# Kernel tuning notes

Measured on AMD Instinct MI355X. Metric: run time of the kernel, lower is better.

The kernel has to match this reference:

```python
import jax, jax.numpy as jnp
import numpy as np

NB_POOLS = 256


def setup_inputs() -> dict:
    key = jax.random.key(0)
    x = jax.random.normal(key, (32, 32, 32, 512), dtype=jnp.float32)
    return {"x": x}


def reference(x) -> jnp.ndarray:
    B, R, C, F = x.shape
    nb_maps = R * C
    x3 = x.reshape(B, nb_maps, F)
    # self-correlation: (B, nb_maps, nb_maps), normalized by feature count
    corr = jnp.einsum('bmf,bnf->bmn', x3, x3) / F
    corr = corr.reshape(B, R, C, nb_maps)
    # percentile ranks into the descending-sorted correlation values
    ranks = jnp.round(jnp.linspace(1.0, nb_maps - 1, NB_POOLS)).astype(jnp.int32)
    # full descending sort along last axis (matches tf.nn.top_k k=nb_maps)
    x_sort = -jnp.sort(-corr, axis=-1)
    x_pool = x_sort[..., ranks]  # (B, R, C, NB_POOLS)
    return x_pool
```

## Files before the change

### kernel.cpp

```cpp
#include <hip/hip_runtime.h>


#define NMAPS 1024
#define FDIM 512
#define TM 16
#define NT 256

typedef __attribute__((ext_vector_type(8))) short short8_t;
typedef __attribute__((ext_vector_type(4))) float f32x4;
typedef _Float16 h2 __attribute__((ext_vector_type(2)));

__device__ __forceinline__ h2 h2min(h2 a, h2 b) { return __builtin_elementwise_min(a, b); }
__device__ __forceinline__ h2 h2max(h2 a, h2 b) { return __builtin_elementwise_max(a, b); }

__device__ __forceinline__ h2 h2swap(h2 v) {
  union { h2 h; unsigned u; } x;
  x.h = v;
  x.u = (x.u >> 16) | (x.u << 16);
  return x.h;
}

__device__ __forceinline__ h2 h2shfl_xor(h2 v, int m) {
  union { h2 h; int i; } u;
  u.h = v;
  u.i = __shfl_xor(u.i, m, 64);
  return u.h;
}

template<int K>
__device__ __forceinline__ void bitonic_stage(h2 w8[8], int lane) {
  const bool laneDesc = (K >= 16) ? ((lane & (K >> 4)) == 0) : true;
#pragma unroll
  for (int j = 512; j >= 16; j >>= 1) {
    if (j > (K >> 1)) continue;
    const int m = j >> 4;
    const bool keepmax = (((lane & m) == 0) == laneDesc);
#pragma unroll
    for (int u = 0; u < 8; ++u) {
      h2 p = h2shfl_xor(w8[u], m);
      h2 mn = h2min(w8[u], p), mx = h2max(w8[u], p);
      w8[u] = keepmax ? mx : mn;
    }
  }
#pragma unroll
  for (int j = 8; j >= 2; j >>= 1) {
    if (j > (K >> 1)) continue;
    const int jw = j >> 1;
#pragma unroll
    for (int u = 0; u < 8; ++u) {
      if ((u & jw) == 0) {
        const int v = u | jw;
        const bool desc = (K <= 8) ? (((2 * u) & K) == 0) : laneDesc;
        h2 mn = h2min(w8[u], w8[v]), mx = h2max(w8[u], w8[v]);
        w8[u] = desc ? mx : mn;
        w8[v] = desc ? mn : mx;
      }
    }
  }
#pragma unroll
  for (int u = 0; u < 8; ++u) {
    const bool desc = (K <= 8) ? (((2 * u) & K) == 0) : laneDesc;
    h2 s = h2swap(w8[u]);
    h2 mn = h2min(w8[u], s), mx = h2max(w8[u], s);
    h2 rd = (h2){mx[0], mn[1]};
    h2 ra = (h2){mn[0], mx[1]};
    w8[u] = desc ? rd : ra;
  }
}

__device__ __forceinline__ void run_bitonic(h2 w8[8], int lane) {
  bitonic_stage<2>(w8, lane);
  bitonic_stage<4>(w8, lane);
  bitonic_stage<8>(w8, lane);
  bitonic_stage<16>(w8, lane);
  bitonic_stage<32>(w8, lane);
  bitonic_stage<64>(w8, lane);
  bitonic_stage<128>(w8, lane);
  bitonic_stage<256>(w8, lane);
  bitonic_stage<512>(w8, lane);
  bitonic_stage<1024>(w8, lane);
}

__global__ __launch_bounds__(256) void cvt_bf16_kernel(const float* __restrict__ x,
                                                       short* __restrict__ xw, int n8) {
  int i = blockIdx.x * 256 + threadIdx.x;
  if (i >= n8) return;
  const float4* x4 = reinterpret_cast<const float4*>(x);
  float4 a = x4[i * 2], c = x4[i * 2 + 1];
  float f[8] = {a.x, a.y, a.z, a.w, c.x, c.y, c.z, c.w};
  union { short8_t v; short s[8]; } o;
#pragma unroll
  for (int j = 0; j < 8; ++j) {
    unsigned u = __float_as_uint(f[j]);
    u += 0x7fffu + ((u >> 16) & 1u);
    o.s[j] = (short)(u >> 16);
  }
  reinterpret_cast<short8_t*>(xw)[i] = o.v;
}

__global__ __launch_bounds__(NT) void corr_gemm_tiled(const short* __restrict__ xw,
                                                      unsigned* __restrict__ corrW) {
  __shared__ short Asm[128 * 32];
  __shared__ short Bsm[128 * 32];
  const int tid = threadIdx.x;
  const int b = blockIdx.y;
  const int it = blockIdx.x >> 3, jt = blockIdx.x & 7;
  const int i0 = it * 128, j0 = jt * 128;
  const int lane = tid & 63;
  const int wid = tid >> 6;
  const int lr = lane & 15;
  const int kg = lane >> 4;
  const int wr = wid >> 1, wc = wid & 1;
  const short* Xb = xw + (size_t)b * NMAPS * FDIM;

  f32x4 acc[4][4];
#pragma unroll
  for (int fm = 0; fm < 4; ++fm)
#pragma unroll
    for (int fn = 0; fn < 4; ++fn) acc[fm][fn] = (f32x4){0.f, 0.f, 0.f, 0.f};

  for (int kt = 0; kt < 16; ++kt) {
    __syncthreads();
#pragma unroll
    for (int rp = 0; rp < 2; ++rp) {
      const int idx = rp * 256 + tid;
      const int r = idx >> 2, s = idx & 3;
      const short* gA = Xb + (size_t)(i0 + r) * FDIM + kt * 32 + s * 8;
      const short* gB = Xb + (size_t)(j0 + r) * FDIM + kt * 32 + s * 8;
      __builtin_amdgcn_global_load_lds(
          (const __attribute__((address_space(1))) unsigned*)gA,
          (__attribute__((address_space(3))) unsigned*)(Asm + idx * 8), 16, 0, 0);
      __builtin_amdgcn_global_load_lds(
          (const __attribute__((address_space(1))) unsigned*)gB,
          (__attribute__((address_space(3))) unsigned*)(Bsm + idx * 8), 16, 0, 0);
    }
    __syncthreads();

    short8_t a[4], bf[4];
#pragma unroll
    for (int fm = 0; fm < 4; ++fm)
      a[fm] = *reinterpret_cast<const short8_t*>(Asm + (wr * 64 + fm * 16 + lr) * 32 + kg * 8);
#pragma unroll
    for (int fn = 0; fn < 4; ++fn)
      bf[fn] = *reinterpret_cast<const short8_t*>(Bsm + (wc * 64 + fn * 16 + lr) * 32 + kg * 8);
#pragma unroll
    for (int fm = 0; fm < 4; ++fm)
#pragma unroll
      for (int fn = 0; fn < 4; ++fn)
        acc[fm][fn] = __builtin_amdgcn_mfma_f32_16x16x32_bf16(bf[fn], a[fm], acc[fm][fn], 0, 0, 0);
  }

#pragma unroll
  for (int fm = 0; fm < 4; ++fm) {
    const size_t roww = ((size_t)b * NMAPS + i0 + wr * 64 + fm * 16 + lr) * 512;
#pragma unroll
    for (int fn = 0; fn < 4; ++fn) {
      h2 lo = (h2){(_Float16)(acc[fm][fn][0] * (1.f / FDIM)),
                   (_Float16)(acc[fm][fn][1] * (1.f / FDIM))};
      h2 hi = (h2){(_Float16)(acc[fm][fn][2] * (1.f / FDIM)),
                   (_Float16)(acc[fm][fn][3] * (1.f / FDIM))};
      const int wq = (j0 + wc * 64 + fn * 16 + kg * 4) >> 1;
      union { h2 h[2]; uint2 u; } pk;
      pk.h[0] = lo; pk.h[1] = hi;
      *reinterpret_cast<uint2*>(corrW + roww + wq) = pk.u;
    }
  }
}

__global__ __launch_bounds__(256) void sort_rows_kernel(const unsigned* __restrict__ corrW,
                                                        float* __restrict__ out) {
  const int tid = threadIdx.x;
  const int lane = tid & 63;
  const int row = blockIdx.x * 4 + (tid >> 6);
  const uint4* r4 = reinterpret_cast<const uint4*>(corrW + (size_t)row * 512);

  h2 w8[8];
  {
    union { uint4 u; h2 h[4]; } a, c;
    a.u = r4[lane * 2];
    c.u = r4[lane * 2 + 1];
    w8[0] = a.h[0]; w8[1] = a.h[1]; w8[2] = a.h[2]; w8[3] = a.h[3];
    w8[4] = c.h[0]; w8[5] = c.h[1]; w8[6] = c.h[2]; w8[7] = c.h[3];
  }

  run_bitonic(w8, lane);

  float* orow = out + (size_t)row * 256;
#pragma unroll
  for (int u = 0; u < 8; ++u) {
#pragma unroll
    for (int hh = 0; hh < 2; ++hh) {
      const int i = lane * 16 + 2 * u + hh;
      const int p = (int)rint((double)(i - 1) * (255.0 / 1022.0));
      const int rk = (int)rint(1.0 + (double)p * (1022.0 / 255.0));
      if (rk == i) orow[p] = (float)w8[u][hh];
    }
  }
}

__global__ __launch_bounds__(NT) void selfcorr_mfma_kernel(const short* __restrict__ xw,
                                                           float* __restrict__ out) {
  __shared__ alignas(16) h2 SH[TM * 512];
  const int tid = threadIdx.x;
  const int b = blockIdx.y;
  const int m0 = blockIdx.x * TM;
  const int lane = tid & 63;
  const int wid = tid >> 6;
  const int lr = lane & 15;
  const int kg = lane >> 4;
  const int wc = wid * 256;
  const short* Xb = xw + (size_t)b * NMAPS * FDIM;

  f32x4 acc[16];
#pragma unroll
  for (int t = 0; t < 16; ++t) acc[t] = (f32x4){0.f, 0.f, 0.f, 0.f};

  for (int kk = 0; kk < 16; ++kk) {
    const short8_t* base = reinterpret_cast<const short8_t*>(Xb + kk * 32 + kg * 8);
    short8_t afrag = base[(size_t)(m0 + lr) * 64];
    short8_t bfrag[16];
#pragma unroll
    for (int t = 0; t < 16; ++t) bfrag[t] = base[(size_t)(wc + t * 16 + lr) * 64];
#pragma unroll
    for (int t = 0; t < 16; ++t)
      acc[t] = __builtin_amdgcn_mfma_f32_16x16x32_bf16(bfrag[t], afrag, acc[t], 0, 0, 0);
  }

  {
    const int xorv = (lr & 7) << 2;
#pragma unroll
    for (int t = 0; t < 16; ++t) {
      h2 lo = (h2){(_Float16)(acc[t][0] * (1.f / FDIM)), (_Float16)(acc[t][1] * (1.f / FDIM))};
      h2 hi = (h2){(_Float16)(acc[t][2] * (1.f / FDIM)), (_Float16)(acc[t][3] * (1.f / FDIM))};
      const int W = (wc >> 1) + t * 8 + kg * 2;
      const int phys = lr * 512 + (W ^ xorv);
      union { h2 h[2]; uint2 u; } pk;
      pk.h[0] = lo; pk.h[1] = hi;
      *reinterpret_cast<uint2*>(&SH[phys]) = pk.u;
    }
  }
  __syncthreads();

  const int rowbase = wid * 4;
  for (int rr = rowbase; rr < rowbase + 4; ++rr) {
    const int rx = (rr & 7) << 2;
    h2 w8[8];
#pragma unroll
    for (int q = 0; q < 2; ++q) {
      const int p4 = rr * 512 + ((lane * 8 + q * 4) ^ rx);
      union { uint4 u; h2 h[4]; } un;
      un.u = *reinterpret_cast<const uint4*>(&SH[p4]);
      w8[q * 4 + 0] = un.h[0]; w8[q * 4 + 1] = un.h[1];
      w8[q * 4 + 2] = un.h[2]; w8[q * 4 + 3] = un.h[3];
    }
    run_bitonic(w8, lane);
#pragma unroll
    for (int q = 0; q < 2; ++q) {
      const int p4 = rr * 512 + ((lane * 8 + q * 4) ^ rx);
      union { uint4 u; h2 h[4]; } un;
      un.h[0] = w8[q * 4 + 0]; un.h[1] = w8[q * 4 + 1];
      un.h[2] = w8[q * 4 + 2]; un.h[3] = w8[q * 4 + 3];
      *reinterpret_cast<uint4*>(&SH[p4]) = un.u;
    }
  }
  __builtin_amdgcn_wave_barrier();

#pragma unroll
  for (int i = 0; i < 16; ++i) {
    const int rr = rowbase + (i >> 2);
    const int p = lane + ((i & 3) << 6);
    const int rank = (int)rint(1.0 + (double)p * (1022.0 / 255.0));
    const int Wr = (rank >> 1) ^ ((rr & 7) << 2);
    h2 hv = SH[rr * 512 + Wr];
    out[((size_t)(b * NMAPS + m0 + rr) << 8) + p] = (float)hv[rank & 1];
  }
}

__device__ __forceinline__ int sw4(int row, int c4) {
  return (row << 8) | (c4 ^ ((c4 >> 3) & 7));
}
__device__ __forceinline__ void ce(float& a, float& b, bool desc) {
  float mn = fminf(a, b);
  float mx = fmaxf(a, b);
  a = desc ? mx : mn;
  b = desc ? mn : mx;
}

__global__ __launch_bounds__(NT) void selfcorr_pool_kernel(const float* __restrict__ x,
                                                           float* __restrict__ out) {
  __shared__ float lds[TM * NMAPS];
  float4* S4 = reinterpret_cast<float4*>(lds);
  const int tid = threadIdx.x;
  const int b = blockIdx.y;
  const int m0 = blockIdx.x * TM;
  const float4* Xb = reinterpret_cast<const float4*>(x) + (size_t)b * NMAPS * (FDIM / 4);

  float4* A4 = reinterpret_cast<float4*>(lds);
#pragma unroll
  for (int idx = tid; idx < TM * (FDIM / 4); idx += NT) {
    A4[idx] = Xb[(m0 + (idx >> 7)) * 128 + (idx & 127)];
  }
  __syncthreads();

  float acc[TM][4];
#pragma unroll
  for (int m = 0; m < TM; ++m)
#pragma unroll
    for (int j = 0; j < 4; ++j) acc[m][j] = 0.0f;

  float4 nb0 = Xb[(tid + 0) * 128];
  float4 nb1 = Xb[(tid + 256) * 128];
  float4 nb2 = Xb[(tid + 512) * 128];
  float4 nb3 = Xb[(tid + 768) * 128];
  for (int k4 = 0; k4 < 128; ++k4) {
    float4 b0 = nb0, b1 = nb1, b2 = nb2, b3 = nb3;
    const int kn = (k4 < 127) ? (k4 + 1) : 127;
    nb0 = Xb[(tid + 0) * 128 + kn];
    nb1 = Xb[(tid + 256) * 128 + kn];
    nb2 = Xb[(tid + 512) * 128 + kn];
    nb3 = Xb[(tid + 768) * 128 + kn];
#pragma unroll
    for (int m = 0; m < TM; ++m) {
      float4 a = A4[m * 128 + k4];
      acc[m][0] += a.x * b0.x + a.y * b0.y + a.z * b0.z + a.w * b0.w;
      acc[m][1] += a.x * b1.x + a.y * b1.y + a.z * b1.z + a.w * b1.w;
      acc[m][2] += a.x * b2.x + a.y * b2.y + a.z * b2.z + a.w * b2.w;
      acc[m][3] += a.x * b3.x + a.y * b3.y + a.z * b3.z + a.w * b3.w;
    }
  }
  __syncthreads();

#pragma unroll
  for (int m = 0; m < TM; ++m) {
#pragma unroll
    for (int j = 0; j < 4; ++j) {
      const int n = tid + (j << 8);
      lds[sw4(m, n >> 2) * 4 + (n & 3)] = acc[m][j] * (1.0f / FDIM);
    }
  }
  __syncthreads();

#pragma unroll
  for (int c = 0; c < 2; ++c) {
    const int cid = tid + (c << 8);
    const int row = cid >> 5;
    const int chunk = cid & 31;
    float r[32];
#pragma unroll
    for (int q = 0; q < 8; ++q) {
      float4 t = S4[sw4(row, (chunk << 3) + q)];
      r[q * 4 + 0] = t.x; r[q * 4 + 1] = t.y; r[q * 4 + 2] = t.z; r[q * 4 + 3] = t.w;
    }
    const bool D = ((chunk & 1) == 0);
#pragma unroll
    for (int k2 = 2; k2 <= 32; k2 <<= 1) {
#pragma unroll
      for (int j = k2 >> 1; j > 0; j >>= 1) {
#pragma unroll
        for (int i = 0; i < 32; ++i) {
          if ((i & j) == 0) ce(r[i], r[i | j], ((i & k2) == 0) ? D : !D);
        }
      }
    }
#pragma unroll
    for (int q = 0; q < 8; ++q) {
      S4[sw4(row, (chunk << 3) + q)] =
          make_float4(r[q * 4 + 0], r[q * 4 + 1], r[q * 4 + 2], r[q * 4 + 3]);
    }
  }
  __syncthreads();

  for (int k = 64; k <= NMAPS; k <<= 1) {
    for (int j = k >> 1; j >= 32; j >>= 1) {
      const int j4 = j >> 2;
      const int kq = k >> 2;
#pragma unroll
      for (int q = 0; q < 8; ++q) {
        const int g = tid + (q << 8);
        const int row = g >> 7;
        const int v = g & 127;
        const int i4 = ((v & ~(j4 - 1)) << 1) | (v & (j4 - 1));
        const bool desc = ((i4 & kq) == 0);
        const int ia = sw4(row, i4);
        const int ib = sw4(row, i4 + j4);
        float4 va = S4[ia];
        float4 vb = S4[ib];
        float4 lo, hi;
        lo.x = fminf(va.x, vb.x); hi.x = fmaxf(va.x, vb.x);
        lo.y = fminf(va.y, vb.y); hi.y = fmaxf(va.y, vb.y);
        lo.z = fminf(va.z, vb.z); hi.z = fmaxf(va.z, vb.z);
        lo.w = fminf(va.w, vb.w); hi.w = fmaxf(va.w, vb.w);
        S4[ia] = desc ? hi : lo;
        S4[ib] = desc ? lo : hi;
      }
      __syncthreads();
    }
#pragma unroll
    for (int c = 0; c < 2; ++c) {
      const int cid = tid + (c << 8);
      const int row = cid >> 5;
      const int chunk = cid & 31;
      const bool D = (((chunk << 5) & k) == 0);
      float r[32];
#pragma unroll
      for (int q = 0; q < 8; ++q) {
        float4 t = S4[sw4(row, (chunk << 3) + q)];
        r[q * 4 + 0] = t.x; r[q * 4 + 1] = t.y; r[q * 4 + 2] = t.z; r[q * 4 + 3] = t.w;
      }
#pragma unroll
      for (int j = 16; j > 0; j >>= 1) {
#pragma unroll
        for (int i = 0; i < 32; ++i) {
          if ((i & j) == 0) ce(r[i], r[i | j], D);
        }
      }
#pragma unroll
      for (int q = 0; q < 8; ++q) {
        S4[sw4(row, (chunk << 3) + q)] =
            make_float4(r[q * 4 + 0], r[q * 4 + 1], r[q * 4 + 2], r[q * 4 + 3]);
      }
    }
    __syncthreads();
  }

  const int p = tid;
  const int rank = (int)rint(1.0 + (double)p * (1022.0 / 255.0));
#pragma unroll
  for (int m = 0; m < TM; ++m) {
    out[((size_t)(b * NMAPS + m0 + m) << 8) + p] = lds[sw4(m, rank >> 2) * 4 + (rank & 3)];
  }
}

extern "C" void kernel_launch(void* const* d_in, const int* in_sizes, int n_in,
                              void* d_out, int out_size, void* d_ws, size_t ws_size,
                              hipStream_t stream) {
  const float* x = reinterpret_cast<const float*>(d_in[0]);
  float* out = reinterpret_cast<float*>(d_out);
  const int nelem = in_sizes[0];
  const int B = nelem / (NMAPS * FDIM);
  const size_t need_split = (size_t)nelem * 2 + (size_t)B * NMAPS * NMAPS * 2;
  if (ws_size >= need_split) {
    short* xw = reinterpret_cast<short*>(d_ws);
    unsigned* corrW = reinterpret_cast<unsigned*>((char*)d_ws + (size_t)nelem * 2);
    const int n8 = nelem / 8;
    hipLaunchKernelGGL(cvt_bf16_kernel, dim3((n8 + 255) / 256), dim3(256), 0, stream, x, xw, n8);
    hipLaunchKernelGGL(corr_gemm_tiled, dim3(64, B), dim3(NT), 0, stream, xw, corrW);
    hipLaunchKernelGGL(sort_rows_kernel, dim3(B * NMAPS / 4), dim3(256), 0, stream, corrW, out);
  } else if (ws_size >= (size_t)nelem * 2) {
    short* xw = reinterpret_cast<short*>(d_ws);
    const int n8 = nelem / 8;
    hipLaunchKernelGGL(cvt_bf16_kernel, dim3((n8 + 255) / 256), dim3(256), 0, stream, x, xw, n8);
    hipLaunchKernelGGL(selfcorr_mfma_kernel, dim3(NMAPS / TM, B), dim3(NT), 0, stream, xw, out);
  } else {
    hipLaunchKernelGGL(selfcorr_pool_kernel, dim3(NMAPS / TM, B), dim3(NT), 0, stream, x, out);
  }
}
```

Measured before the change: 186.7 us.

## Presort 64-element runs in GEMM epilogue and skip early bitonic stages in sort kernel

The GEMM epilogue now runs the first bitonic stages (up to 64-element runs) on the accumulator registers, using cross-lane shuffles among the kg lanes. It then stores 16 contiguous sorted halves per lane with wider stores. The row-sort kernel starts at stage 128, which removes the early stages from the sort pass. The epilogue uses perm-based compare-exchange helpers. The cost is extra ALU work and register pressure in the GEMM kernel, and correctness depends on the lane-to-column mapping matching the sort layout.

Result: faster. 169.9 us (-9.0%).

```diff
diff --git a/kernel.cpp b/kernel.cpp
--- a/kernel.cpp
+++ b/kernel.cpp
@@ -10,14 +10,18 @@
 typedef __attribute__((ext_vector_type(4))) float f32x4;
 typedef _Float16 h2 __attribute__((ext_vector_type(2)));
 
+#define SELD 0x03020504u
+#define SELA 0x07060100u
+
 __device__ __forceinline__ h2 h2min(h2 a, h2 b) { return __builtin_elementwise_min(a, b); }
 __device__ __forceinline__ h2 h2max(h2 a, h2 b) { return __builtin_elementwise_max(a, b); }
 
+__device__ __forceinline__ unsigned h2u(h2 x) { union { h2 h; unsigned u; } t; t.h = x; return t.u; }
+__device__ __forceinline__ h2 u2h(unsigned x) { union { h2 h; unsigned u; } t; t.u = x; return t.h; }
+
 __device__ __forceinline__ h2 h2swap(h2 v) {
-  union { h2 h; unsigned u; } x;
-  x.h = v;
-  x.u = (x.u >> 16) | (x.u << 16);
-  return x.h;
+  unsigned u = h2u(v);
+  return u2h((u >> 16) | (u << 16));
 }
 
 __device__ __forceinline__ h2 h2shfl_xor(h2 v, int m) {
@@ -25,6 +29,54 @@
   u.h = v;
   u.i = __shfl_xor(u.i, m, 64);
   return u.h;
+}
+
+__device__ __forceinline__ void ce_pair(h2& a, h2& b, bool d) {
+  h2 mn = h2min(a, b), mx = h2max(a, b);
+  a = d ? mx : mn;
+  b = d ? mn : mx;
+}
+
+__device__ __forceinline__ h2 ce1(h2 w, unsigned sel) {
+  h2 s = h2swap(w);
+  h2 mn = h2min(w, s), mx = h2max(w, s);
+#if __has_builtin(__builtin_amdgcn_perm)
+  return u2h(__builtin_amdgcn_perm(h2u(mx), h2u(mn), sel));
+#else
+  h2 rd; rd[0] = mx[0]; rd[1] = mn[1];
+  h2 ra; ra[0] = mn[0]; ra[1] = mx[1];
+  return (sel == SELD) ? rd : ra;
+#endif
+}
+
+__device__ __forceinline__ void intra_merge16(h2 w[8], bool d, unsigned sel) {
+  ce_pair(w[0], w[4], d); ce_pair(w[1], w[5], d); ce_pair(w[2], w[6], d); ce_pair(w[3], w[7], d);
+  ce_pair(w[0], w[2], d); ce_pair(w[1], w[3], d); ce_pair(w[4], w[6], d); ce_pair(w[5], w[7], d);
+  ce_pair(w[0], w[1], d); ce_pair(w[2], w[3], d); ce_pair(w[4], w[5], d); ce_pair(w[6], w[7], d);
+#pragma unroll
+  for (int u = 0; u < 8; ++u) w[u] = ce1(w[u], sel);
+}
+
+__device__ __forceinline__ void sort16(h2 w[8], bool d, unsigned sd, unsigned si) {
+  w[0] = ce1(w[0], sd); w[1] = ce1(w[1], si); w[2] = ce1(w[2], sd); w[3] = ce1(w[3], si);
+  w[4] = ce1(w[4], sd); w[5] = ce1(w[5], si); w[6] = ce1(w[6], sd); w[7] = ce1(w[7], si);
+  ce_pair(w[0], w[1], d); ce_pair(w[2], w[3], !d); ce_pair(w[4], w[5], d); ce_pair(w[6], w[7], !d);
+  w[0] = ce1(w[0], sd); w[1] = ce1(w[1], sd); w[2] = ce1(w[2], si); w[3] = ce1(w[3], si);
+  w[4] = ce1(w[4], sd); w[5] = ce1(w[5], sd); w[6] = ce1(w[6], si); w[7] = ce1(w[7], si);
+  ce_pair(w[0], w[2], d); ce_pair(w[1], w[3], d); ce_pair(w[4], w[6], !d); ce_pair(w[5], w[7], !d);
+  ce_pair(w[0], w[1], d); ce_pair(w[2], w[3], d); ce_pair(w[4], w[5], !d); ce_pair(w[6], w[7], !d);
+  w[0] = ce1(w[0], sd); w[1] = ce1(w[1], sd); w[2] = ce1(w[2], sd); w[3] = ce1(w[3], sd);
+  w[4] = ce1(w[4], si); w[5] = ce1(w[5], si); w[6] = ce1(w[6], si); w[7] = ce1(w[7], si);
+  intra_merge16(w, d, sd);
+}
+
+__device__ __forceinline__ void cross_ce(h2 w[8], int m, bool keepmax) {
+#pragma unroll
+  for (int u = 0; u < 8; ++u) {
+    h2 p = h2shfl_xor(w[u], m);
+    h2 mn = h2min(w[u], p), mx = h2max(w[u], p);
+    w[u] = keepmax ? mx : mn;
+  }
 }
 
 template<int K>
@@ -66,6 +118,18 @@
     h2 ra = (h2){mn[0], mx[1]};
     w8[u] = desc ? rd : ra;
   }
+}
+
+template<int K>
+__device__ __forceinline__ void bitonic_stage_tail(h2 w8[8], int lane) {
+  const bool laneDesc = ((lane & (K >> 4)) == 0);
+#pragma unroll
+  for (int j = 512; j >= 16; j >>= 1) {
+    if (j > (K >> 1)) continue;
+    const int m = j >> 4;
+    cross_ce(w8, m, ((lane & m) == 0) == laneDesc);
+  }
+  intra_merge16(w8, laneDesc, laneDesc ? SELD : SELA);
 }
 
 __device__ __forceinline__ void run_bitonic(h2 w8[8], int lane) {
@@ -150,20 +214,33 @@
         acc[fm][fn] = __builtin_amdgcn_mfma_f32_16x16x32_bf16(bf[fn], a[fm], acc[fm][fn], 0, 0, 0);
   }
 
+  const bool D0 = (wc == 0);
+  const bool d16 = ((kg & 1) == 0) ? D0 : !D0;
+  const unsigned sd16 = d16 ? SELD : SELA, si16 = d16 ? SELA : SELD;
+  const bool d32 = ((kg & 2) == 0) ? D0 : !D0;
+  const float sc = 1.f / FDIM;
+
 #pragma unroll
   for (int fm = 0; fm < 4; ++fm) {
+    h2 w[8];
+#pragma unroll
+    for (int fn = 0; fn < 4; ++fn) {
+      w[2 * fn] = (h2){(_Float16)(acc[fm][fn][0] * sc), (_Float16)(acc[fm][fn][1] * sc)};
+      w[2 * fn + 1] = (h2){(_Float16)(acc[fm][fn][2] * sc), (_Float16)(acc[fm][fn][3] * sc)};
+    }
+    sort16(w, d16, sd16, si16);
+    cross_ce(w, 16, ((kg & 1) == 0) == d32);
+    intra_merge16(w, d32, d32 ? SELD : SELA);
+    cross_ce(w, 32, ((kg & 2) == 0) == D0);
+    cross_ce(w, 16, ((kg & 1) == 0) == D0);
+    intra_merge16(w, D0, D0 ? SELD : SELA);
     const size_t roww = ((size_t)b * NMAPS + i0 + wr * 64 + fm * 16 + lr) * 512;
-#pragma unroll
-    for (int fn = 0; fn < 4; ++fn) {
-      h2 lo = (h2){(_Float16)(acc[fm][fn][0] * (1.f / FDIM)),
-                   (_Float16)(acc[fm][fn][1] * (1.f / FDIM))};
-      h2 hi = (h2){(_Float16)(acc[fm][fn][2] * (1.f / FDIM)),
-                   (_Float16)(acc[fm][fn][3] * (1.f / FDIM))};
-      const int wq = (j0 + wc * 64 + fn * 16 + kg * 4) >> 1;
-      union { h2 h[2]; uint2 u; } pk;
-      pk.h[0] = lo; pk.h[1] = hi;
-      *reinterpret_cast<uint2*>(corrW + roww + wq) = pk.u;
-    }
+    const int wq = (j0 >> 1) + wc * 32 + kg * 8;
+    union { h2 h[4]; uint4 u; } s0, s1;
+    s0.h[0] = w[0]; s0.h[1] = w[1]; s0.h[2] = w[2]; s0.h[3] = w[3];
+    s1.h[0] = w[4]; s1.h[1] = w[5]; s1.h[2] = w[6]; s1.h[3] = w[7];
+    *reinterpret_cast<uint4*>(corrW + roww + wq) = s0.u;
+    *reinterpret_cast<uint4*>(corrW + roww + wq + 4) = s1.u;
   }
 }
 
@@ -183,7 +260,10 @@
     w8[4] = c.h[0]; w8[5] = c.h[1]; w8[6] = c.h[2]; w8[7] = c.h[3];
   }
 
-  run_bitonic(w8, lane);
+  bitonic_stage_tail<128>(w8, lane);
+  bitonic_stage_tail<256>(w8, lane);
+  bitonic_stage_tail<512>(w8, lane);
+  bitonic_stage_tail<1024>(w8, lane);
 
   float* orow = out + (size_t)row * 256;
 #pragma unroll
```
